# Kernel optimization log

Hardware: AMD Instinct MI355X
Metric: run time of the kernel (lower is better)

Reference implementation:

```python
import jax, jax.numpy as jnp
import numpy as np

GROUPS = 32
N_HEADS = 16
EPS = 1e-5


def setup_inputs() -> dict:
    key = jax.random.key(0)
    ks = jax.random.split(key, 5)
    b, c, t = 4, 1024, 1024
    return {
        "x": jax.random.normal(ks[0], (b, c, t), dtype=jnp.float32),
        "gn_weight": jnp.ones((c,), dtype=jnp.float32),
        "gn_bias": jnp.zeros((c,), dtype=jnp.float32),
        "qkv_w": jax.random.normal(ks[1], (3 * c, c), dtype=jnp.float32) * (c ** -0.5),
        "qkv_b": jax.random.normal(ks[2], (3 * c,), dtype=jnp.float32) * 0.02,
        "proj_w": jax.random.normal(ks[3], (c, c), dtype=jnp.float32) * (c ** -0.5),
        "proj_b": jax.random.normal(ks[4], (c,), dtype=jnp.float32) * 0.02,
    }


def _group_norm(x, weight, bias):
    # x: [b, c, t]; GroupNorm32 computes stats in float32 (already fp32 here)
    b, c, t = x.shape
    xg = x.reshape(b, GROUPS, c // GROUPS, t)
    mean = xg.mean(axis=(2, 3), keepdims=True)
    var = xg.var(axis=(2, 3), keepdims=True)
    xn = ((xg - mean) * jax.lax.rsqrt(var + EPS)).reshape(b, c, t)
    return xn * weight[None, :, None] + bias[None, :, None]


def reference(x, gn_weight, gn_bias, qkv_w, qkv_b, proj_w, proj_b):
    b, c, t = x.shape
    xn = _group_norm(x, gn_weight, gn_bias)
    # 1x1 Conv1d == channel matmul: [3c, c] x [b, c, t] -> [b, 3c, t]
    qkv = jnp.einsum('oc,bct->bot', qkv_w, xn) + qkv_b[None, :, None]
    ch = c // N_HEADS
    # legacy per-head interleaved layout: reshape to [b*H, 3*ch, t], split
    qkv = qkv.reshape(b * N_HEADS, 3 * ch, t)
    q, k, v = qkv[:, :ch], qkv[:, ch:2 * ch], qkv[:, 2 * ch:]
    scale = ch ** -0.25  # 1/sqrt(sqrt(ch)), applied to both q and k
    weight = jnp.einsum('bct,bcs->bts', q * scale, k * scale)  # [b*H, t, t]
    weight = jax.nn.softmax(weight.astype(jnp.float32), axis=-1).astype(weight.dtype)
    a = jnp.einsum('bts,bcs->bct', weight, v).reshape(b, c, t)
    h = jnp.einsum('oc,bct->bot', proj_w, a) + proj_b[None, :, None]
    return x + h
```

## Files before the change

kernel.cpp:

```cpp
#include <hip/hip_runtime.h>
#include <hip/hip_bf16.h>

typedef __bf16 bf16;
typedef __bf16 bf16x2 __attribute__((ext_vector_type(2)));
typedef __bf16 bf16x4 __attribute__((ext_vector_type(4)));
typedef __bf16 bf16x8 __attribute__((ext_vector_type(8)));
typedef float  f32x4  __attribute__((ext_vector_type(4)));
typedef float  f32x16 __attribute__((ext_vector_type(16)));

static __device__ __forceinline__ f32x4 mfma16(bf16x8 a, bf16x8 b, f32x4 c) {
  return __builtin_amdgcn_mfma_f32_16x16x32_bf16(a, b, c, 0, 0, 0);
}
static __device__ __forceinline__ f32x16 mfma32(bf16x8 a, bf16x8 b, f32x16 c) {
  return __builtin_amdgcn_mfma_f32_32x32x16_bf16(a, b, c, 0, 0, 0);
}

static __device__ __forceinline__ void gload_lds16(const bf16* g, bf16* l) {
  __builtin_amdgcn_global_load_lds(
      (const __attribute__((address_space(1))) void*)g,
      (__attribute__((address_space(3))) void*)l, 16, 0, 0);
}

static __device__ __forceinline__ int cvtpk(float lo, float hi) {
  int w;
  asm("v_cvt_pk_bf16_f32 %0, %1, %2" : "=v"(w) : "v"(lo), "v"(hi));
  return w;
}
static __device__ __forceinline__ void plswap(int& x, int& y) {
  asm("v_permlane32_swap_b32 %0, %1" : "+v"(x), "+v"(y));
}

#define VMCNT0() asm volatile("s_waitcnt vmcnt(0)" ::: "memory")
#define VMCNT2() asm volatile("s_waitcnt vmcnt(2)" ::: "memory")
#define VMCNT4() asm volatile("s_waitcnt vmcnt(4)" ::: "memory")
#define BARRIER()                                        \
  do {                                                   \
    asm volatile("" ::: "memory");                       \
    __builtin_amdgcn_s_barrier();                        \
    asm volatile("" ::: "memory");                       \
  } while (0)

__global__ __launch_bounds__(512) void pre_kernel(const float* __restrict__ x,
                                                  const float* __restrict__ gw,
                                                  const float* __restrict__ gb,
                                                  bf16* __restrict__ xnT,
                                                  const float* __restrict__ qkv_w,
                                                  bf16* __restrict__ wq,
                                                  const float* __restrict__ proj_w,
                                                  bf16* __restrict__ wp) {
  int blk = blockIdx.x;
  int tid = threadIdx.x;
  if (blk >= 512) {
    int i = (blk - 512) * 512 + tid;
    const int na4 = 3072 * 1024 / 4;
    const float* src; bf16* dst;
    if (i < na4) { src = qkv_w; dst = wq; }
    else         { src = proj_w; dst = wp; i -= na4; }
    float4 v = ((const float4*)src)[i];
    bf16x4 o = { (bf16)v.x, (bf16)v.y, (bf16)v.z, (bf16)v.w };
    *(bf16x4*)(dst + 4ll * i) = o;
    return;
  }
  int id = blk;
  int b = id >> 7, g = (id >> 2) & 31, qtr = id & 3;
  const float* xb = x + ((size_t)b * 1024 + g * 32) * 1024;
  float s = 0.f, sq = 0.f;
  const float4* x4 = (const float4*)xb;
  for (int i = tid; i < 8192; i += 512) {
    float4 v = x4[i];
    s  += v.x + v.y + v.z + v.w;
    sq += v.x * v.x + v.y * v.y + v.z * v.z + v.w * v.w;
  }
#pragma unroll
  for (int off = 32; off; off >>= 1) { s += __shfl_down(s, off); sq += __shfl_down(sq, off); }
  __shared__ float red[16];
  int wv = tid >> 6;
  if ((tid & 63) == 0) { red[wv] = s; red[8 + wv] = sq; }
  __syncthreads();
  s = 0.f; sq = 0.f;
#pragma unroll
  for (int i = 0; i < 8; ++i) { s += red[i]; sq += red[8 + i]; }
  float mean = s * (1.f / 32768.f);
  float var  = sq * (1.f / 32768.f) - mean * mean;
  float rstd = rsqrtf(var + 1e-5f);

  __shared__ bf16 tile[64][36];
  int c = tid >> 4, q = tid & 15;
  int r = tid >> 3, q2 = tid & 7;
  float wc = gw[g * 32 + c] * rstd;
  float fb = gb[g * 32 + c] - mean * wc;
  for (int t0 = qtr * 256; t0 < qtr * 256 + 256; t0 += 64) {
    float4 v = *(const float4*)(xb + (size_t)c * 1024 + t0 + q * 4);
    tile[q * 4 + 0][c] = (bf16)(v.x * wc + fb);
    tile[q * 4 + 1][c] = (bf16)(v.y * wc + fb);
    tile[q * 4 + 2][c] = (bf16)(v.z * wc + fb);
    tile[q * 4 + 3][c] = (bf16)(v.w * wc + fb);
    __syncthreads();
    *(bf16x4*)&xnT[((size_t)b * 1024 + t0 + r) * 1024 + g * 32 + q2 * 4] =
        *(bf16x4*)&tile[r][q2 * 4];
    __syncthreads();
  }
}

__global__ __launch_bounds__(512, 1) void qkv_kernel(
    const bf16* __restrict__ A, const bf16* __restrict__ Bw,
    const float* __restrict__ bias,
    bf16* __restrict__ qkT, bf16* __restrict__ vC) {
  extern __shared__ __align__(16) bf16 smem[];

  int tid = threadIdx.x, wid = tid >> 6, lane = tid & 63;
  int l15 = lane & 15, l4 = lane >> 4;
  int wr = wid >> 2, wc = wid & 3;
  int rsw = (l15 & 7) << 4;

  int sid = (blockIdx.x & 7) * 32 + (blockIdx.x >> 3);
  int bx = sid & 15, by = (sid >> 4) & 3, z = sid >> 6;
  int m0 = by * 256, n0 = bx * 192;
  const bf16* Ab = A + (size_t)z * 1024 * 1024 + (size_t)m0 * 1024;
  const bf16* Bb = Bw + (size_t)n0 * 1024;

  int srow = tid >> 3;
  int csw  = (tid & 7) ^ (srow & 7);
  auto stageA = [&](int d, int kt) {
    bf16* dst = smem + d * 16384;
    const bf16* src = Ab + kt * 64 + csw * 8;
#pragma unroll
    for (int hh = 0; hh < 2; ++hh)
#pragma unroll
      for (int L = 0; L < 2; ++L)
        gload_lds16(src + (size_t)(hh * 128 + L * 64 + srow) * 1024,
                    dst + hh * 8192 + (L * 512 + wid * 64) * 8);
  };
  auto stageB = [&](int d, int kt) {
    bf16* dst = smem + 49152 + d * 12288;
    const bf16* src = Bb + kt * 64 + csw * 8;
#pragma unroll
    for (int L = 0; L < 3; ++L)
      gload_lds16(src + (size_t)(L * 64 + srow) * 1024, dst + (L * 512 + wid * 64) * 8);
  };

  f32x4 acc[8][3] = {};

  auto compute = [&](int ta, int tb) {
    const char* Ab8 = (const char*)smem + ta * 32768 + wr * 16384;
    const char* Bb8 = (const char*)smem + 98304 + tb * 24576;
    bf16x8 bfr[3][2], af[4][2];
#pragma unroll
    for (int ni = 0; ni < 3; ++ni) {
      int rb = (wc * 48 + ni * 16 + l15) * 128;
#pragma unroll
      for (int kk = 0; kk < 2; ++kk)
        bfr[ni][kk] = *(const bf16x8*)(Bb8 + rb + ((kk * 64 + l4 * 16) ^ rsw));
    }
#pragma unroll
    for (int mi = 0; mi < 4; ++mi) {
      int rb = (mi * 16 + l15) * 128;
#pragma unroll
      for (int kk = 0; kk < 2; ++kk)
        af[mi][kk] = *(const bf16x8*)(Ab8 + rb + ((kk * 64 + l4 * 16) ^ rsw));
    }
#pragma unroll
    for (int mi = 0; mi < 4; ++mi)
#pragma unroll
      for (int ni = 0; ni < 3; ++ni)
#pragma unroll
        for (int kk = 0; kk < 2; ++kk)
          acc[mi][ni] = mfma16(af[mi][kk], bfr[ni][kk], acc[mi][ni]);
#pragma unroll
    for (int mi = 0; mi < 4; ++mi) {
      int rb = ((4 + mi) * 16 + l15) * 128;
#pragma unroll
      for (int kk = 0; kk < 2; ++kk)
        af[mi][kk] = *(const bf16x8*)(Ab8 + rb + ((kk * 64 + l4 * 16) ^ rsw));
    }
#pragma unroll
    for (int mi = 0; mi < 4; ++mi)
#pragma unroll
      for (int ni = 0; ni < 3; ++ni)
#pragma unroll
        for (int kk = 0; kk < 2; ++kk)
          acc[4 + mi][ni] = mfma16(af[mi][kk], bfr[ni][kk], acc[4 + mi][ni]);
  };

  stageA(0, 0); stageB(0, 0); stageA(1, 1);
  VMCNT4();
  BARRIER();

  for (int t = 0; t < 14; ++t) {
    stageB((t + 1) & 1, t + 1);
    stageA((t + 2) % 3, t + 2);
    compute(t % 3, t & 1);
    VMCNT4();
    BARRIER();
  }
  stageB(1, 15);
  compute(2, 0);
  VMCNT0();
  BARRIER();
  compute(0, 1);

  const float scale = 0.35355339059327373f;
  int h = bx;
#pragma unroll
  for (int ni = 0; ni < 3; ++ni) {
    int oin = wc * 48 + ni * 16;
    float bv = bias[n0 + oin + l15];
#pragma unroll
    for (int mi = 0; mi < 8; ++mi) {
      int tb = m0 + wr * 128 + mi * 16 + l4 * 4;
      f32x4 v = acc[mi][ni];
      if (oin < 128) {
#pragma unroll
        for (int i = 0; i < 4; ++i)
          qkT[((size_t)z * 1024 + tb + i) * 2048 + h * 128 + oin + l15] =
              (bf16)((v[i] + bv) * scale);
      } else {
        bf16x4 st = { (bf16)(v[0] + bv), (bf16)(v[1] + bv),
                      (bf16)(v[2] + bv), (bf16)(v[3] + bv) };
        *(bf16x4*)&vC[(((size_t)z * 16 + h) * 64 + (oin - 128 + l15)) * 1024 + tb] = st;
      }
    }
  }
}

__global__ __launch_bounds__(512, 1) void proj_kernel(
    const bf16* __restrict__ A, const bf16* __restrict__ Bw,
    const float* __restrict__ bias,
    const float* __restrict__ xres, float* __restrict__ out) {
  extern __shared__ __align__(16) bf16 smem[];

  int tid = threadIdx.x, wid = tid >> 6, lane = tid & 63;
  int l15 = lane & 15, l4 = lane >> 4;
  int wr = wid >> 2, wc = wid & 3;
  int rsw = (l15 & 7) << 4;

  int sid = (blockIdx.x & 7) * 32 + (blockIdx.x >> 3);
  int bx = sid & 7, by = (sid >> 3) & 7, z = sid >> 6;
  int m0 = by * 128, n0 = bx * 128;
  const bf16* Ab = A + (size_t)z * 1024 * 1024 + (size_t)m0 * 1024;
  const bf16* Bb = Bw + (size_t)n0 * 1024;

  int srow = tid >> 3;
  int csw  = (tid & 7) ^ (srow & 7);
  auto stageA = [&](int d, int kt) {
    bf16* dst = smem + d * 8192;
    const bf16* src = Ab + kt * 64 + csw * 8;
#pragma unroll
    for (int L = 0; L < 2; ++L)
      gload_lds16(src + (size_t)(L * 64 + srow) * 1024, dst + (L * 512 + wid * 64) * 8);
  };
  auto stageB = [&](int d, int kt) {
    bf16* dst = smem + 24576 + d * 8192;
    const bf16* src = Bb + kt * 64 + csw * 8;
#pragma unroll
    for (int L = 0; L < 2; ++L)
      gload_lds16(src + (size_t)(L * 64 + srow) * 1024, dst + (L * 512 + wid * 64) * 8);
  };

  f32x4 acc[4][2] = {};

  auto compute = [&](int ta, int tb) {
    const char* Ab8 = (const char*)smem + ta * 16384 + wr * 8192;
    const char* Bb8 = (const char*)smem + 49152 + tb * 16384;
    bf16x8 bfr[2][2], af[4][2];
#pragma unroll
    for (int ni = 0; ni < 2; ++ni) {
      int rb = (wc * 32 + ni * 16 + l15) * 128;
#pragma unroll
      for (int kk = 0; kk < 2; ++kk)
        bfr[ni][kk] = *(const bf16x8*)(Bb8 + rb + ((kk * 64 + l4 * 16) ^ rsw));
    }
#pragma unroll
    for (int mi = 0; mi < 4; ++mi) {
      int rb = (mi * 16 + l15) * 128;
#pragma unroll
      for (int kk = 0; kk < 2; ++kk)
        af[mi][kk] = *(const bf16x8*)(Ab8 + rb + ((kk * 64 + l4 * 16) ^ rsw));
    }
#pragma unroll
    for (int mi = 0; mi < 4; ++mi)
#pragma unroll
      for (int ni = 0; ni < 2; ++ni)
#pragma unroll
        for (int kk = 0; kk < 2; ++kk)
          acc[mi][ni] = mfma16(af[mi][kk], bfr[ni][kk], acc[mi][ni]);
  };

  stageA(0, 0); stageB(0, 0); stageA(1, 1);
  VMCNT2();
  BARRIER();

  for (int t = 0; t < 14; ++t) {
    stageB((t + 1) & 1, t + 1);
    stageA((t + 2) % 3, t + 2);
    compute(t % 3, t & 1);
    VMCNT2();
    BARRIER();
  }
  stageB(1, 15);
  compute(2, 0);
  VMCNT0();
  BARRIER();
  compute(0, 1);

#pragma unroll
  for (int ni = 0; ni < 2; ++ni) {
    int o = n0 + wc * 32 + ni * 16 + l15;
    float bv = bias[o];
#pragma unroll
    for (int mi = 0; mi < 4; ++mi) {
      int tb = m0 + wr * 64 + mi * 16 + l4 * 4;
      size_t base = ((size_t)z * 1024 + o) * 1024 + tb;
      float4 xr = *(const float4*)(xres + base);
      f32x4 v = acc[mi][ni];
      float4 ov = { xr.x + v[0] + bv, xr.y + v[1] + bv,
                    xr.z + v[2] + bv, xr.w + v[3] + bv };
      *(float4*)(out + base) = ov;
    }
  }
}

__global__ __launch_bounds__(256, 3) void attn_kernel(const bf16* __restrict__ qkT,
                                                      const bf16* __restrict__ vC,
                                                      bf16* __restrict__ aT) {
  __shared__ __align__(16) bf16 Kt[2][64 * 64];
  __shared__ __align__(16) bf16 Vt[2][64 * 64];

  int id = blockIdx.x;
  int sid = (id & 7) * 64 + (id >> 3);
  int head = sid >> 3, tblk = sid & 7;
  int b = head >> 4, h = head & 15;
  int t0 = tblk * 128;
  int tid = threadIdx.x, wid = tid >> 6, lane = tid & 63;
  int l31 = lane & 31, hi = lane >> 5;
  int trow = t0 + wid * 32;

  const bf16* kbase = qkT + (size_t)b * 1024 * 2048 + h * 128 + 64;
  const bf16* vbase = vC + (size_t)(b * 16 + h) * 64 * 1024;
  int rsw = (lane & 7) << 4;

  const bf16* qrow = qkT + ((size_t)b * 1024 + trow + l31) * 2048 + h * 128;
  bf16x8 qf[4];
#pragma unroll
  for (int kb = 0; kb < 4; ++kb) qf[kb] = *(const bf16x8*)(qrow + kb * 16 + hi * 8);

  int rl = lane >> 3;
  int scol = (((lane & 7) * 16) ^ (rl << 4)) >> 1;
  auto stage = [&](int buf, int st) {
    int s0 = st * 64;
#pragma unroll
    for (int j = 0; j < 2; ++j) {
      int g8 = wid * 2 + j;
      int r = g8 * 8 + rl;
      gload_lds16(kbase + (size_t)(s0 + r) * 2048 + scol, &Kt[buf][g8 * 512]);
      gload_lds16(vbase + (size_t)r * 1024 + s0 + scol, &Vt[buf][g8 * 512]);
    }
  };

  float m_run = -1e30f, l_run = 0.f;
  f32x16 oacc[2] = {};

  stage(0, 0);
  __syncthreads();

  for (int st = 0; st < 16; ++st) {
    int cur = st & 1;
    if (st < 15) stage(cur ^ 1, st + 1);

    const char* Kb = (const char*)Kt[cur];
    f32x16 sf[2] = {};
    __builtin_amdgcn_s_setprio(1);
#pragma unroll
    for (int sb = 0; sb < 2; ++sb) {
      int rowb = (sb * 32 + l31) * 128;
#pragma unroll
      for (int kb = 0; kb < 4; ++kb) {
        bf16x8 kf = *(const bf16x8*)(Kb + rowb + ((kb * 32 + hi * 16) ^ rsw));
        sf[sb] = mfma32(kf, qf[kb], sf[sb]);
      }
    }
    __builtin_amdgcn_s_setprio(0);

    float mb;
    {
      float m0v = fmaxf(sf[0][0], sf[0][1]);
#pragma unroll
      for (int r = 2; r < 16; ++r) m0v = fmaxf(m0v, sf[0][r]);
#pragma unroll
      for (int r = 0; r < 16; ++r) m0v = fmaxf(m0v, sf[1][r]);
      mb = m0v;
    }
    mb = fmaxf(mb, __shfl_xor(mb, 32));
    if (!__all(mb - m_run <= 8.f)) {
      float mn = fmaxf(m_run, mb);
      float corr = __expf(m_run - mn);
      m_run = mn;
      l_run *= corr;
#pragma unroll
      for (int cb = 0; cb < 2; ++cb)
#pragma unroll
        for (int r = 0; r < 16; ++r) oacc[cb][r] *= corr;
    }

    float sbsum = 0.f;
    bf16x8 pf[4];
#pragma unroll
    for (int sb = 0; sb < 2; ++sb) {
      float p[16];
#pragma unroll
      for (int r = 0; r < 16; ++r) {
        p[r] = __expf(sf[sb][r] - m_run);
        sbsum += p[r];
      }
      int w0 = cvtpk(p[0], p[1]),   w1 = cvtpk(p[2], p[3]);
      int w2 = cvtpk(p[4], p[5]),   w3 = cvtpk(p[6], p[7]);
      int w4 = cvtpk(p[8], p[9]),   w5 = cvtpk(p[10], p[11]);
      int w6 = cvtpk(p[12], p[13]), w7 = cvtpk(p[14], p[15]);
      plswap(w0, w2); plswap(w1, w3);
      plswap(w4, w6); plswap(w5, w7);
      int4 f0 = { w0, w1, w2, w3 };
      int4 f1 = { w4, w5, w6, w7 };
      pf[sb * 2 + 0] = *(bf16x8*)&f0;
      pf[sb * 2 + 1] = *(bf16x8*)&f1;
    }
    sbsum += __shfl_xor(sbsum, 32);
    l_run += sbsum;

    const char* Vb = (const char*)Vt[cur];
    __builtin_amdgcn_s_setprio(1);
#pragma unroll
    for (int ks = 0; ks < 4; ++ks) {
#pragma unroll
      for (int cb = 0; cb < 2; ++cb) {
        bf16x8 vf = *(const bf16x8*)(Vb + (cb * 32 + l31) * 128 + ((ks * 32 + hi * 16) ^ rsw));
        oacc[cb] = mfma32(vf, pf[ks], oacc[cb]);
      }
    }
    __builtin_amdgcn_s_setprio(0);
    __syncthreads();
  }

  float rdiv = 1.f / l_run;
  int t = trow + l31;
#pragma unroll
  for (int cb = 0; cb < 2; ++cb) {
#pragma unroll
    for (int q = 0; q < 4; ++q) {
      bf16x4 ov = { (bf16)(oacc[cb][q * 4 + 0] * rdiv), (bf16)(oacc[cb][q * 4 + 1] * rdiv),
                    (bf16)(oacc[cb][q * 4 + 2] * rdiv), (bf16)(oacc[cb][q * 4 + 3] * rdiv) };
      int c0 = h * 64 + cb * 32 + hi * 4 + q * 8;
      *(bf16x4*)&aT[((size_t)b * 1024 + t) * 1024 + c0] = ov;
    }
  }
}

extern "C" void kernel_launch(void* const* d_in, const int* in_sizes, int n_in,
                              void* d_out, int out_size, void* d_ws, size_t ws_size,
                              hipStream_t stream) {
  const float* x      = (const float*)d_in[0];
  const float* gw     = (const float*)d_in[1];
  const float* gb     = (const float*)d_in[2];
  const float* qkv_w  = (const float*)d_in[3];
  const float* qkv_b  = (const float*)d_in[4];
  const float* proj_w = (const float*)d_in[5];
  const float* proj_b = (const float*)d_in[6];
  float* out = (float*)d_out;

  char* ws = (char*)d_ws;
  bf16* wq_bf = (bf16*)(ws);
  bf16* wp_bf = (bf16*)(ws + 6ll  * 1024 * 1024);
  bf16* xnT   = (bf16*)(ws + 8ll  * 1024 * 1024);
  bf16* qkT   = (bf16*)(ws + 16ll * 1024 * 1024);
  bf16* vC    = (bf16*)(ws + 32ll * 1024 * 1024);
  bf16* aT    = (bf16*)(ws + 40ll * 1024 * 1024);

  hipFuncSetAttribute(reinterpret_cast<const void*>(qkv_kernel),
                      hipFuncAttributeMaxDynamicSharedMemorySize, 147456);
  hipFuncSetAttribute(reinterpret_cast<const void*>(proj_kernel),
                      hipFuncAttributeMaxDynamicSharedMemorySize, 81920);

  pre_kernel<<<dim3(2560), dim3(512), 0, stream>>>(x, gw, gb, xnT, qkv_w, wq_bf, proj_w, wp_bf);
  qkv_kernel<<<dim3(256), dim3(512), 147456, stream>>>(xnT, wq_bf, qkv_b, qkT, vC);
  attn_kernel<<<dim3(512), dim3(256), 0, stream>>>(qkT, vC, aT);
  proj_kernel<<<dim3(256), dim3(512), 81920, stream>>>(aT, wp_bf, proj_b, x, out);
}
```

Measured before the change: 96.52 us.

## Halve QKV GEMM tile rows and double-buffer to fit two blocks per CU

The QKV projection GEMM tile shrinks from 256x192 to 128x192, doubling the grid to 512 blocks. Shared memory drops from 144KB to 80KB and launch bounds allow two blocks per CU. The triple-buffered A and double-buffered B pipeline with partial vmcnt waits becomes a plain double buffer that waits for all loads each iteration. This aims for more occupancy and better spread across CUs, at the cost of less reuse per tile, more total B traffic and a shallower prefetch pipeline.

```diff
diff --git a/kernel.cpp b/kernel.cpp
--- a/kernel.cpp
+++ b/kernel.cpp
@@ -31,8 +31,6 @@
 }
 
 #define VMCNT0() asm volatile("s_waitcnt vmcnt(0)" ::: "memory")
-#define VMCNT2() asm volatile("s_waitcnt vmcnt(2)" ::: "memory")
-#define VMCNT4() asm volatile("s_waitcnt vmcnt(4)" ::: "memory")
 #define BARRIER()                                        \
   do {                                                   \
     asm volatile("" ::: "memory");                       \
@@ -102,7 +100,7 @@
   }
 }
 
-__global__ __launch_bounds__(512, 1) void qkv_kernel(
+__global__ __launch_bounds__(512, 2) void qkv_kernel(
     const bf16* __restrict__ A, const bf16* __restrict__ Bw,
     const float* __restrict__ bias,
     bf16* __restrict__ qkT, bf16* __restrict__ vC) {
@@ -113,37 +111,34 @@
   int wr = wid >> 2, wc = wid & 3;
   int rsw = (l15 & 7) << 4;
 
-  int sid = (blockIdx.x & 7) * 32 + (blockIdx.x >> 3);
-  int bx = sid & 15, by = (sid >> 4) & 3, z = sid >> 6;
-  int m0 = by * 256, n0 = bx * 192;
+  int sid = (blockIdx.x & 7) * 64 + (blockIdx.x >> 3);
+  int bx = sid & 15, by = (sid >> 4) & 7, z = sid >> 7;
+  int m0 = by * 128, n0 = bx * 192;
   const bf16* Ab = A + (size_t)z * 1024 * 1024 + (size_t)m0 * 1024;
   const bf16* Bb = Bw + (size_t)n0 * 1024;
 
   int srow = tid >> 3;
   int csw  = (tid & 7) ^ (srow & 7);
   auto stageA = [&](int d, int kt) {
-    bf16* dst = smem + d * 16384;
+    bf16* dst = smem + d * 8192;
     const bf16* src = Ab + kt * 64 + csw * 8;
 #pragma unroll
-    for (int hh = 0; hh < 2; ++hh)
-#pragma unroll
-      for (int L = 0; L < 2; ++L)
-        gload_lds16(src + (size_t)(hh * 128 + L * 64 + srow) * 1024,
-                    dst + hh * 8192 + (L * 512 + wid * 64) * 8);
+    for (int L = 0; L < 2; ++L)
+      gload_lds16(src + (size_t)(L * 64 + srow) * 1024, dst + (L * 512 + wid * 64) * 8);
   };
   auto stageB = [&](int d, int kt) {
-    bf16* dst = smem + 49152 + d * 12288;
+    bf16* dst = smem + 16384 + d * 12288;
     const bf16* src = Bb + kt * 64 + csw * 8;
 #pragma unroll
     for (int L = 0; L < 3; ++L)
       gload_lds16(src + (size_t)(L * 64 + srow) * 1024, dst + (L * 512 + wid * 64) * 8);
   };
 
-  f32x4 acc[8][3] = {};
-
-  auto compute = [&](int ta, int tb) {
-    const char* Ab8 = (const char*)smem + ta * 32768 + wr * 16384;
-    const char* Bb8 = (const char*)smem + 98304 + tb * 24576;
+  f32x4 acc[4][3] = {};
+
+  auto compute = [&](int d) {
+    const char* Ab8 = (const char*)smem + d * 16384 + wr * 8192;
+    const char* Bb8 = (const char*)smem + 32768 + d * 24576;
     bf16x8 bfr[3][2], af[4][2];
 #pragma unroll
     for (int ni = 0; ni < 3; ++ni) {
@@ -166,38 +161,19 @@
 #pragma unroll
         for (int kk = 0; kk < 2; ++kk)
           acc[mi][ni] = mfma16(af[mi][kk], bfr[ni][kk], acc[mi][ni]);
-#pragma unroll
-    for (int mi = 0; mi < 4; ++mi) {
-      int rb = ((4 + mi) * 16 + l15) * 128;
-#pragma unroll
-      for (int kk = 0; kk < 2; ++kk)
-        af[mi][kk] = *(const bf16x8*)(Ab8 + rb + ((kk * 64 + l4 * 16) ^ rsw));
-    }
-#pragma unroll
-    for (int mi = 0; mi < 4; ++mi)
-#pragma unroll
-      for (int ni = 0; ni < 3; ++ni)
-#pragma unroll
-        for (int kk = 0; kk < 2; ++kk)
-          acc[4 + mi][ni] = mfma16(af[mi][kk], bfr[ni][kk], acc[4 + mi][ni]);
-  };
-
-  stageA(0, 0); stageB(0, 0); stageA(1, 1);
-  VMCNT4();
-  BARRIER();
-
-  for (int t = 0; t < 14; ++t) {
-    stageB((t + 1) & 1, t + 1);
-    stageA((t + 2) % 3, t + 2);
-    compute(t % 3, t & 1);
-    VMCNT4();
-    BARRIER();
-  }
-  stageB(1, 15);
-  compute(2, 0);
+  };
+
+  stageA(0, 0); stageB(0, 0);
   VMCNT0();
   BARRIER();
-  compute(0, 1);
+
+  for (int t = 0; t < 16; ++t) {
+    int d = t & 1;
+    if (t < 15) { stageB(d ^ 1, t + 1); stageA(d ^ 1, t + 1); }
+    compute(d);
+    VMCNT0();
+    BARRIER();
+  }
 
   const float scale = 0.35355339059327373f;
   int h = bx;
@@ -206,8 +182,8 @@
     int oin = wc * 48 + ni * 16;
     float bv = bias[n0 + oin + l15];
 #pragma unroll
-    for (int mi = 0; mi < 8; ++mi) {
-      int tb = m0 + wr * 128 + mi * 16 + l4 * 4;
+    for (int mi = 0; mi < 4; ++mi) {
+      int tb = m0 + wr * 64 + mi * 16 + l4 * 4;
       f32x4 v = acc[mi][ni];
       if (oin < 128) {
 #pragma unroll
@@ -223,6 +199,7 @@
   }
 }
 
+#define VMCNT2() asm volatile("s_waitcnt vmcnt(2)" ::: "memory")
 __global__ __launch_bounds__(512, 1) void proj_kernel(
     const bf16* __restrict__ A, const bf16* __restrict__ Bw,
     const float* __restrict__ bias,
@@ -475,12 +452,12 @@
   bf16* aT    = (bf16*)(ws + 40ll * 1024 * 1024);
 
   hipFuncSetAttribute(reinterpret_cast<const void*>(qkv_kernel),
-                      hipFuncAttributeMaxDynamicSharedMemorySize, 147456);
+                      hipFuncAttributeMaxDynamicSharedMemorySize, 81920);
   hipFuncSetAttribute(reinterpret_cast<const void*>(proj_kernel),
                       hipFuncAttributeMaxDynamicSharedMemorySize, 81920);
 
   pre_kernel<<<dim3(2560), dim3(512), 0, stream>>>(x, gw, gb, xnT, qkv_w, wq_bf, proj_w, wp_bf);
-  qkv_kernel<<<dim3(256), dim3(512), 147456, stream>>>(xnT, wq_bf, qkv_b, qkT, vC);
+  qkv_kernel<<<dim3(512), dim3(512), 81920, stream>>>(xnT, wq_bf, qkv_b, qkT, vC);
   attn_kernel<<<dim3(512), dim3(256), 0, stream>>>(qkT, vC, aT);
   proj_kernel<<<dim3(256), dim3(512), 81920, stream>>>(aT, wp_bf, proj_b, x, out);
 }
```

After: 93.93 us. -2.7%, faster.
